# Optimization experiments

Hardware: AMD Instinct MI355X
Metric: run time of the kernel (lower is better)

## Reference

```python
import jax, jax.numpy as jnp
import numpy as np

NUM_GRAPHS = 16
MAX_NODES = 256
EMB_DIM = 64
EDGES_PER_GRAPH = 4096


def setup_inputs() -> dict:
    rng = np.random.default_rng(0)
    src_list, dst_list = [], []
    for g in range(NUM_GRAPHS):
        # distinct off-diagonal (src,dst) pairs per graph (simple directed graph, no self loops)
        flat = rng.choice(MAX_NODES * MAX_NODES, size=EDGES_PER_GRAPH + MAX_NODES, replace=False)
        s, d = flat // MAX_NODES, flat % MAX_NODES
        keep = s != d
        s, d = s[keep][:EDGES_PER_GRAPH], d[keep][:EDGES_PER_GRAPH]
        off = g * MAX_NODES
        src_list.append(s + off)
        dst_list.append(d + off)
    edge_index = jnp.asarray(
        np.stack([np.concatenate(src_list), np.concatenate(dst_list)]), dtype=jnp.int32)
    batch_vec = jnp.repeat(jnp.arange(NUM_GRAPHS, dtype=jnp.int32), MAX_NODES)
    k1, k2 = jax.random.split(jax.random.key(0))
    edge_attr = jax.random.normal(k1, (NUM_GRAPHS * EDGES_PER_GRAPH, EMB_DIM), jnp.float32)
    emb_table = jax.random.normal(k2, (3, EMB_DIM), jnp.float32)
    return {"edge_attr": edge_attr, "emb_table": emb_table,
            "edge_index": edge_index, "batch_vec": batch_vec}


def reference(edge_attr, emb_table, edge_index, batch_vec):
    B, N, D = NUM_GRAPHS, MAX_NODES, edge_attr.shape[-1]
    # per-graph node offsets (pyG-style, from the batch vector)
    counts = jax.ops.segment_sum(jnp.ones_like(batch_vec), batch_vec, num_segments=B)
    starts = jnp.cumsum(counts) - counts  # first global node index of each graph
    src, dst = edge_index[0], edge_index[1]
    g = batch_vec[src]
    ls = src - starts[g]  # local row index
    ld = dst - starts[g]  # local col index
    # to_dense_adj with edge_attr: scatter-add edge features -> [B, N, N, D]
    edge_dense = jnp.zeros((B, N, N, D), edge_attr.dtype).at[g, ls, ld].add(edge_attr)
    # edge types: scatter 2 at edges, add_self_loops fill 1 on the diagonal
    t = jnp.zeros((B, N, N), jnp.int32).at[g, ls, ld].add(2)
    node = jnp.arange(batch_vec.shape[0], dtype=jnp.int32)
    gn = batch_vec
    ln = node - starts[gn]
    t = t.at[gn, ln, ln].add(1)
    A = 2 - t  # 0 = connected, 1 = diagonal, 2 = disconnected/padding
    table = emb_table.at[0].set(0.0)  # padding_idx=0 -> zero vector for connected pairs
    return edge_dense + table[A]
```

## Files before the change

kernel.cpp:

```cpp
#include <hip/hip_runtime.h>

#define NB 16
#define NN 256
#define ND 64
#define EPG 4096
#define NE (NB*EPG)
#define NNODE (NB*NN)
#define MAXE_ROW 256

typedef float f4 __attribute__((ext_vector_type(4)));
typedef int   i4 __attribute__((ext_vector_type(4)));

__global__ __launch_bounds__(256) void fill_kernel(const float* __restrict__ emb,
                                                   f4* __restrict__ out) {
    constexpr int nth    = 256 * 256;
    constexpr int total4 = NB * NN * NN * (ND / 4);
    const int tid = blockIdx.x * 256 + threadIdx.x;
    const f4 v2 = ((const f4*)(emb + 2 * ND))[threadIdx.x & 15];
    #pragma unroll 16
    for (int i = 0; i < total4 / nth; ++i)
        out[tid + i * nth] = v2;
}

__global__ __launch_bounds__(256) void row_patch(const float* __restrict__ edge_attr,
                                                 const int* __restrict__ edge_index,
                                                 const float* __restrict__ emb,
                                                 f4* __restrict__ out) {
    __shared__ int lcnt;
    __shared__ int llist[MAXE_ROW];
    const int row = blockIdx.x;
    const int g   = row >> 8;
    const int tid = threadIdx.x;

    if (tid == 0) lcnt = 0;
    __syncthreads();

    const i4* __restrict__ srcv = (const i4*)(edge_index + g * EPG);
    #pragma unroll
    for (int k = 0; k < 4; ++k) {
        const int vi = tid + k * 256;
        const i4 s = srcv[vi];
        #pragma unroll
        for (int j = 0; j < 4; ++j) {
            if (s[j] == row) {
                const int e  = g * EPG + vi * 4 + j;
                const int ld = edge_index[NE + e] & (NN - 1);
                const int p  = atomicAdd(&lcnt, 1);
                llist[p] = (e << 8) | ld;
            }
        }
    }
    __syncthreads();

    const int dq = tid & 15;
    f4* __restrict__ rowout = out + (long)row * NN * (ND / 4);

    if (tid < 16)
        rowout[(row & (NN - 1)) * (ND / 4) + tid] = ((const f4*)(emb + 1 * ND))[tid];

    const int cnt = lcnt;
    for (int k = tid >> 4; k < cnt; k += 16) {
        const int pk = llist[k];
        const int e  = pk >> 8;
        const int ld = pk & 255;
        rowout[ld * (ND / 4) + dq] =
            __builtin_nontemporal_load((const f4*)edge_attr + (long)e * (ND / 4) + dq);
    }
}

extern "C" void kernel_launch(void* const* d_in, const int* in_sizes, int n_in,
                              void* d_out, int out_size, void* d_ws, size_t ws_size,
                              hipStream_t stream) {
    const float* edge_attr  = (const float*)d_in[0];
    const float* emb_table  = (const float*)d_in[1];
    const int*   edge_index = (const int*)d_in[2];
    f4* out = (f4*)d_out;

    fill_kernel<<<256, 256, 0, stream>>>(emb_table, out);
    row_patch<<<NNODE, 256, 0, stream>>>(edge_attr, edge_index, emb_table, out);
}
```

Measured before the change: 61.08 us.

## Fuse background fill and edge patching into one kernel over 16-row spans

Merges the fill kernel and the per-row patch kernel into a single kernel where each block owns 16 consecutive rows. The block scans its graph's edges once for all 16 rows, fills its span with the disconnected embedding, then writes the diagonal and edge features. This drops one launch and cuts the repeated edge-index scanning, which was done once per row, by a factor of 16. The cost is a larger shared list of 16KB and only 256 blocks, so each block carries a much bigger write load. Ordering between the fill and the patch writes relies on the __syncthreads between them.

```diff
diff --git a/kernel.cpp b/kernel.cpp
--- a/kernel.cpp
+++ b/kernel.cpp
@@ -6,31 +6,23 @@
 #define EPG 4096
 #define NE (NB*EPG)
 #define NNODE (NB*NN)
-#define MAXE_ROW 256
+#define RPB 16
+#define GRID (NNODE/RPB)
+#define SPAN_F4 (RPB*NN*(ND/4))
+#define MAXE_SPAN 4096
 
 typedef float f4 __attribute__((ext_vector_type(4)));
 typedef int   i4 __attribute__((ext_vector_type(4)));
 
-__global__ __launch_bounds__(256) void fill_kernel(const float* __restrict__ emb,
-                                                   f4* __restrict__ out) {
-    constexpr int nth    = 256 * 256;
-    constexpr int total4 = NB * NN * NN * (ND / 4);
-    const int tid = blockIdx.x * 256 + threadIdx.x;
-    const f4 v2 = ((const f4*)(emb + 2 * ND))[threadIdx.x & 15];
-    #pragma unroll 16
-    for (int i = 0; i < total4 / nth; ++i)
-        out[tid + i * nth] = v2;
-}
-
-__global__ __launch_bounds__(256) void row_patch(const float* __restrict__ edge_attr,
-                                                 const int* __restrict__ edge_index,
-                                                 const float* __restrict__ emb,
-                                                 f4* __restrict__ out) {
+__global__ __launch_bounds__(256) void fused_kernel(const float* __restrict__ edge_attr,
+                                                    const int* __restrict__ edge_index,
+                                                    const float* __restrict__ emb,
+                                                    f4* __restrict__ out) {
     __shared__ int lcnt;
-    __shared__ int llist[MAXE_ROW];
-    const int row = blockIdx.x;
-    const int g   = row >> 8;
-    const int tid = threadIdx.x;
+    __shared__ int llist[MAXE_SPAN];
+    const int tid  = threadIdx.x;
+    const int row0 = blockIdx.x * RPB;
+    const int g    = row0 >> 8;
 
     if (tid == 0) lcnt = 0;
     __syncthreads();
@@ -42,28 +34,37 @@
         const i4 s = srcv[vi];
         #pragma unroll
         for (int j = 0; j < 4; ++j) {
-            if (s[j] == row) {
+            const int lrow = s[j] - row0;
+            if ((unsigned)lrow < RPB) {
                 const int e  = g * EPG + vi * 4 + j;
                 const int ld = edge_index[NE + e] & (NN - 1);
                 const int p  = atomicAdd(&lcnt, 1);
-                llist[p] = (e << 8) | ld;
+                llist[p] = (e << 12) | (lrow << 8) | ld;
             }
         }
     }
+
+    f4* __restrict__ spanout = out + (long)row0 * NN * (ND / 4);
+    const f4 v2 = ((const f4*)(emb + 2 * ND))[tid & 15];
+    #pragma unroll 16
+    for (int i = 0; i < SPAN_F4 / 256; ++i)
+        spanout[tid + i * 256] = v2;
+
     __syncthreads();
 
     const int dq = tid & 15;
-    f4* __restrict__ rowout = out + (long)row * NN * (ND / 4);
-
-    if (tid < 16)
-        rowout[(row & (NN - 1)) * (ND / 4) + tid] = ((const f4*)(emb + 1 * ND))[tid];
-
+    if (tid < RPB * 16) {
+        const int lrow = tid >> 4;
+        const int col  = (row0 + lrow) & (NN - 1);
+        spanout[(lrow * NN + col) * (ND / 4) + dq] = ((const f4*)(emb + 1 * ND))[dq];
+    }
     const int cnt = lcnt;
     for (int k = tid >> 4; k < cnt; k += 16) {
-        const int pk = llist[k];
-        const int e  = pk >> 8;
-        const int ld = pk & 255;
-        rowout[ld * (ND / 4) + dq] =
+        const int pk   = llist[k];
+        const int e    = pk >> 12;
+        const int lrow = (pk >> 8) & 15;
+        const int ld   = pk & 255;
+        spanout[(lrow * NN + ld) * (ND / 4) + dq] =
             __builtin_nontemporal_load((const f4*)edge_attr + (long)e * (ND / 4) + dq);
     }
 }
@@ -76,6 +77,5 @@
     const int*   edge_index = (const int*)d_in[2];
     f4* out = (f4*)d_out;
 
-    fill_kernel<<<256, 256, 0, stream>>>(emb_table, out);
-    row_patch<<<NNODE, 256, 0, stream>>>(edge_attr, edge_index, emb_table, out);
+    fused_kernel<<<GRID, 256, 0, stream>>>(edge_attr, edge_index, emb_table, out);
 }
```

After: 61.14 us. About the same (+0.1%).
